# Optimization experiments

Hardware: AMD Instinct MI355X
Metric: run time of the kernel (lower is better)

The kernel has to match this reference:

```python
import jax, jax.numpy as jnp
import numpy as np

D_MODEL = 1024
N_HEAD = 16
D_K = D_MODEL // N_HEAD


def setup_inputs() -> dict:
    key = jax.random.key(0)
    ks = jax.random.split(key, 11)
    B, S, D = 2, 2048, D_MODEL
    scale = 1.0 / np.sqrt(D)
    inp = {
        "q": jax.random.normal(ks[0], (B, S, D), jnp.float32),
        "k": jax.random.normal(ks[1], (B, S, D), jnp.float32),
        "v": jax.random.normal(ks[2], (B, S, D), jnp.float32),
        "w_q": jax.random.normal(ks[3], (D, D), jnp.float32) * scale,
        "b_q": jnp.zeros((D,), jnp.float32),
        "w_k": jax.random.normal(ks[4], (D, D), jnp.float32) * scale,
        "b_k": jnp.zeros((D,), jnp.float32),
        "w_v": jax.random.normal(ks[5], (D, D), jnp.float32) * scale,
        "b_v": jnp.zeros((D,), jnp.float32),
        "w_o": jax.random.normal(ks[6], (D, D), jnp.float32) * scale,
        "b_o": jnp.zeros((D,), jnp.float32),
    }
    return inp


def _split_heads(x):
    # torch: chunk(n_head, dim=-1) then cat(dim=0) -> [H*B, S, d_k]
    B, S, D = x.shape
    x = x.reshape(B, S, N_HEAD, D_K)            # contiguous last-dim chunks
    return x.transpose(2, 0, 1, 3).reshape(N_HEAD * B, S, D_K)


def _merge_heads(x, B):
    # torch: chunk(n_head, dim=0) then cat(dim=-1) -> [B, S, D]
    HB, S, dk = x.shape
    x = x.reshape(N_HEAD, B, S, dk).transpose(1, 2, 0, 3)
    return x.reshape(B, S, N_HEAD * dk)


def reference(q, k, v, w_q, b_q, w_k, b_k, w_v, b_v, w_o, b_o):
    B = q.shape[0]
    qh = _split_heads(q @ w_q + b_q)            # [H*B, S, d_k]
    kh = _split_heads(k @ w_k + b_k)
    vh = _split_heads(v @ w_v + b_v)
    # scaled dot-product attention (naive, materializes scores)
    scores = jnp.einsum('bqd,bkd->bqk', qh, kh) / jnp.sqrt(jnp.float32(D_K))
    attn = jax.nn.softmax(scores, axis=-1)
    out = jnp.einsum('bqk,bkd->bqd', attn, vh)  # [H*B, S, d_k]
    out = _merge_heads(out, B)                  # [B, S, D]
    return out @ w_o + b_o
```

## Files before the change

### kernel.cpp

```cpp
#include <hip/hip_runtime.h>
#include <hip/hip_bf16.h>
#include <stdint.h>

#define DEVINL __device__ __forceinline__

typedef __attribute__((ext_vector_type(8))) short bf16x8;
typedef __attribute__((ext_vector_type(4))) short short4v;
typedef __attribute__((ext_vector_type(8))) unsigned short ushort8;
typedef __attribute__((ext_vector_type(4))) float f32x4;
typedef __attribute__((ext_vector_type(16))) float f32x16;

DEVINL unsigned short f2bf(float x) {
  union { float f; uint32_t u; } v; v.f = x;
  uint32_t u = v.u;
  u += 0x7fffu + ((u >> 16) & 1u);
  return (unsigned short)(u >> 16);
}

DEVINL uint32_t pack_bf16x2(float lo, float hi) {
  __hip_bfloat162 bb = __float22bfloat162_rn(make_float2(lo, hi));
  uint32_t r;
  __builtin_memcpy(&r, &bb, 4);
  return r;
}

DEVINL void gload_lds16(const void* g, void* l) {
  __builtin_amdgcn_global_load_lds((const __attribute__((address_space(1))) void*)g,
                                   (__attribute__((address_space(3))) void*)l, 16, 0, 0);
}

#define E2(x) __builtin_amdgcn_exp2f(x)

__global__ void cvt3_f32_bf16(const float* __restrict__ in0, unsigned short* __restrict__ out0,
                              const float* __restrict__ in1, unsigned short* __restrict__ out1,
                              const float* __restrict__ in2, unsigned short* __restrict__ out2,
                              int nper) {
  int nblk = gridDim.x / 3;
  int which = blockIdx.x / nblk;
  int i = ((blockIdx.x % nblk) * blockDim.x + threadIdx.x) * 8;
  if (i >= nper) return;
  const float* in = which == 0 ? in0 : which == 1 ? in1 : in2;
  unsigned short* out = which == 0 ? out0 : which == 1 ? out1 : out2;
  float4 a = *(const float4*)(in + i);
  float4 b = *(const float4*)(in + i + 4);
  ushort8 r;
  r[0] = f2bf(a.x); r[1] = f2bf(a.y); r[2] = f2bf(a.z); r[3] = f2bf(a.w);
  r[4] = f2bf(b.x); r[5] = f2bf(b.y); r[6] = f2bf(b.z); r[7] = f2bf(b.w);
  *(ushort8*)(out + i) = r;
}

__global__ __launch_bounds__(256) void transpose_w4(
    const float* __restrict__ w0, unsigned short* __restrict__ o0,
    const float* __restrict__ w1, unsigned short* __restrict__ o1,
    const float* __restrict__ w2, unsigned short* __restrict__ o2,
    const float* __restrict__ w3, unsigned short* __restrict__ o3) {
  __shared__ float tile[64][65];
  int z = blockIdx.z;
  const float* w = z == 0 ? w0 : z == 1 ? w1 : z == 2 ? w2 : w3;
  unsigned short* wt = z == 0 ? o0 : z == 1 ? o1 : z == 2 ? o2 : o3;
  int k0 = blockIdx.y * 64, n0 = blockIdx.x * 64;
  int t = threadIdx.x;
  for (int i = 0; i < 4; ++i) {
    int r = (t >> 4) + i * 16;
    int c = (t & 15) * 4;
    float4 v = *(const float4*)(w + (size_t)(k0 + r) * 1024 + n0 + c);
    tile[r][c] = v.x; tile[r][c + 1] = v.y; tile[r][c + 2] = v.z; tile[r][c + 3] = v.w;
  }
  __syncthreads();
  for (int i = 0; i < 4; ++i) {
    int rn = (t >> 4) + i * 16;
    int ck = (t & 15) * 4;
    short4v o;
    o[0] = (short)f2bf(tile[ck + 0][rn]);
    o[1] = (short)f2bf(tile[ck + 1][rn]);
    o[2] = (short)f2bf(tile[ck + 2][rn]);
    o[3] = (short)f2bf(tile[ck + 3][rn]);
    *(short4v*)(wt + (size_t)(n0 + rn) * 1024 + k0 + ck) = o;
  }
}

DEVINL void gemm_body(const unsigned short* __restrict__ A,
                      const unsigned short* __restrict__ Bt,
                      const float* __restrict__ bias,
                      void* __restrict__ out, float scale, int mode,
                      int bx, int by) {
  constexpr int K = 1024;
  __shared__ unsigned short Alds[2 * 128 * 32];
  __shared__ unsigned short Blds[2 * 64 * 32];
  int tile_m = bx * 128;
  int tile_n = by * 64;
  int t = threadIdx.x, lane = t & 63, wid = t >> 6;
  int wm = wid >> 1, wn = wid & 1;
  int fr = lane & 15, fq = lane >> 4;
  f32x4 acc[4][2] = {};

  int ga0 = wid * 64 + lane, ga1 = ga0 + 256;
  int gb0 = wid * 64 + lane;
  int ra0 = ga0 >> 2, ca0 = ((ga0 & 3) ^ ((ra0 >> 1) & 3)) * 8;
  int ra1 = ga1 >> 2, ca1 = ((ga1 & 3) ^ ((ra1 >> 1) & 3)) * 8;
  int rb0 = gb0 >> 2, cb0 = ((gb0 & 3) ^ ((rb0 >> 1) & 3)) * 8;
  const unsigned short* Abase = A  + (size_t)tile_m * K;
  const unsigned short* Bbase = Bt + (size_t)tile_n * K;

  int aoff[4], boff[2];
#pragma unroll
  for (int i = 0; i < 4; ++i) {
    int r = wm * 64 + i * 16 + fr;
    aoff[i] = (r * 4 + (fq ^ ((r >> 1) & 3))) * 8;
  }
#pragma unroll
  for (int j = 0; j < 2; ++j) {
    int r = wn * 32 + j * 16 + fr;
    boff[j] = (r * 4 + (fq ^ ((r >> 1) & 3))) * 8;
  }

  auto stage = [&](int nb, int k0) {
    gload_lds16(Abase + (size_t)ra0 * K + k0 + ca0, Alds + nb * 4096 + ga0 * 8);
    gload_lds16(Abase + (size_t)ra1 * K + k0 + ca1, Alds + nb * 4096 + ga1 * 8);
    gload_lds16(Bbase + (size_t)rb0 * K + k0 + cb0, Blds + nb * 2048 + gb0 * 8);
  };
  auto compute = [&](int nb) {
    bf16x8 af[4], bfb[2];
#pragma unroll
    for (int i = 0; i < 4; ++i) af[i] = *(const bf16x8*)(Alds + nb * 4096 + aoff[i]);
#pragma unroll
    for (int j = 0; j < 2; ++j) bfb[j] = *(const bf16x8*)(Blds + nb * 2048 + boff[j]);
#pragma unroll
    for (int i = 0; i < 4; ++i)
#pragma unroll
      for (int j = 0; j < 2; ++j)
        acc[i][j] = __builtin_amdgcn_mfma_f32_16x16x32_bf16(af[i], bfb[j], acc[i][j], 0, 0, 0);
  };

  stage(0, 0);
  __syncthreads();
  for (int it = 0; it < 16; ++it) {
    int k1 = (2 * it + 1) * 32, k2 = (2 * it + 2) * 32;
    stage(1, k1);
    compute(0);
    __syncthreads();
    if (k2 < K) stage(0, k2);
    compute(1);
    __syncthreads();
  }

#pragma unroll
  for (int i = 0; i < 4; ++i) {
#pragma unroll
    for (int j = 0; j < 2; ++j) {
      int n = tile_n + wn * 32 + j * 16 + fr;
      float bv = bias[n];
      int m0 = tile_m + wm * 64 + i * 16 + fq * 4;
      if (mode == 0) {
        size_t base = (size_t)((n >> 6) * 2 + (m0 >> 11)) * (2048 * 64) + (n & 63);
#pragma unroll
        for (int r = 0; r < 4; ++r)
          ((unsigned short*)out)[base + (size_t)((m0 + r) & 2047) * 64] =
              f2bf((acc[i][j][r] + bv) * scale);
      } else if (mode == 2) {
        size_t base = (size_t)((n >> 6) * 2 + (m0 >> 11)) * (64 * 2048)
                    + (size_t)(n & 63) * 2048 + (m0 & 2047);
        short4v o;
#pragma unroll
        for (int r = 0; r < 4; ++r) o[r] = (short)f2bf(acc[i][j][r] + bv);
        *(short4v*)((unsigned short*)out + base) = o;
      } else {
#pragma unroll
        for (int r = 0; r < 4; ++r)
          ((float*)out)[(size_t)(m0 + r) * 1024 + n] = acc[i][j][r] + bv;
      }
    }
  }
}

__global__ __launch_bounds__(256) void gemm_qkv(
    const unsigned short* __restrict__ Xq, const unsigned short* __restrict__ Xk,
    const unsigned short* __restrict__ Xv,
    const unsigned short* __restrict__ Wtq, const unsigned short* __restrict__ Wtk,
    const unsigned short* __restrict__ Wtv,
    const float* __restrict__ bq, const float* __restrict__ bk,
    const float* __restrict__ bv,
    unsigned short* __restrict__ Qh, unsigned short* __restrict__ Kh,
    unsigned short* __restrict__ Vt, float qscale) {
  int z = blockIdx.z;
  const unsigned short* A  = z == 0 ? Xq : z == 1 ? Xk : Xv;
  const unsigned short* Bt = z == 0 ? Wtq : z == 1 ? Wtk : Wtv;
  const float* bias        = z == 0 ? bq : z == 1 ? bk : bv;
  void* out                = z == 0 ? (void*)Qh : z == 1 ? (void*)Kh : (void*)Vt;
  float scale = z == 0 ? qscale : 1.0f;
  int mode = z == 2 ? 2 : 0;
  gemm_body(A, Bt, bias, out, scale, mode, blockIdx.x, blockIdx.y);
}

__global__ __launch_bounds__(256) void gemm_o(
    const unsigned short* __restrict__ A, const unsigned short* __restrict__ Bt,
    const float* __restrict__ bias, float* __restrict__ out) {
  gemm_body(A, Bt, bias, out, 1.0f, 1, blockIdx.x, blockIdx.y);
}

__global__ __launch_bounds__(256) void attn_fwd(
    const unsigned short* __restrict__ Qh,
    const unsigned short* __restrict__ Kh,
    const unsigned short* __restrict__ Vtg,
    unsigned short* __restrict__ O) {
  constexpr int S = 2048, DK = 64;
  __shared__ unsigned short Klds[2 * 64 * 64];
  __shared__ unsigned short Vlds[2 * 64 * 64];
  __shared__ unsigned short Plds[4 * 32 * 72];

  int wg = blockIdx.x;
  int swz = (wg & 7) * 64 + (wg >> 3);
  int hb = swz >> 4;
  int qt = swz & 15;
  int t = threadIdx.x, lane = t & 63, wid = t >> 6;
  int lq = lane & 31, hi = lane >> 5;
  int q0 = qt * 128;

  const unsigned short* Qb = Qh  + (size_t)hb * S * DK;
  const unsigned short* Kb = Kh  + (size_t)hb * S * DK;
  const unsigned short* Vb = Vtg + (size_t)hb * DK * S;

  bf16x8 qf[4];
#pragma unroll
  for (int kk = 0; kk < 4; ++kk)
    qf[kk] = *(const bf16x8*)(Qb + (size_t)(q0 + wid * 32 + lq) * DK + kk * 16 + hi * 8);

  int g0 = wid * 128 + lane, g1 = g0 + 64;
  int sr0 = g0 >> 3, sc0 = ((g0 & 7) ^ (sr0 & 7)) * 8;
  int sr1 = g1 >> 3, sc1 = ((g1 & 7) ^ (sr1 & 7)) * 8;

  int koff[2][4], voff[2][4];
#pragma unroll
  for (int h2 = 0; h2 < 2; ++h2) {
    int row = 32 * h2 + lq;
#pragma unroll
    for (int kk = 0; kk < 4; ++kk)
      koff[h2][kk] = (row * 8 + ((2 * kk + hi) ^ (row & 7))) * 8;
  }
#pragma unroll
  for (int jt = 0; jt < 2; ++jt) {
    int row = 32 * jt + lq;
#pragma unroll
    for (int ks = 0; ks < 4; ++ks)
      voff[jt][ks] = (row * 8 + ((2 * ks + hi) ^ (row & 7))) * 8;
  }

  unsigned short* Pw = Plds + wid * (32 * 72) + lq * 72;

  auto stage = [&](int nb, int kt) {
    const unsigned short* Ksrc = Kb + (size_t)kt * 64 * DK;
    const unsigned short* Vsrc = Vb + (size_t)kt * 64;
    gload_lds16(Ksrc + sr0 * 64 + sc0, Klds + nb * 4096 + g0 * 8);
    gload_lds16(Ksrc + sr1 * 64 + sc1, Klds + nb * 4096 + g1 * 8);
    gload_lds16(Vsrc + (size_t)sr0 * S + sc0, Vlds + nb * 4096 + g0 * 8);
    gload_lds16(Vsrc + (size_t)sr1 * S + sc1, Vlds + nb * 4096 + g1 * 8);
  };

  float m = -INFINITY, l = 0.f;
  f32x16 oacc[2] = {};

  auto tilestep = [&](int nb) {
    const unsigned short* Kc = Klds + nb * 4096;
    const unsigned short* Vc = Vlds + nb * 4096;

    f32x16 sacc[2] = {};
#pragma unroll
    for (int kk = 0; kk < 4; ++kk) {
      bf16x8 k0 = *(const bf16x8*)(Kc + koff[0][kk]);
      sacc[0] = __builtin_amdgcn_mfma_f32_32x32x16_bf16(k0, qf[kk], sacc[0], 0, 0, 0);
      bf16x8 k1 = *(const bf16x8*)(Kc + koff[1][kk]);
      sacc[1] = __builtin_amdgcn_mfma_f32_32x32x16_bf16(k1, qf[kk], sacc[1], 0, 0, 0);
    }

    float pmax = fmaxf(sacc[0][0], sacc[0][1]);
#pragma unroll
    for (int r = 2; r < 16; r += 2) pmax = fmaxf(pmax, fmaxf(sacc[0][r], sacc[0][r + 1]));
#pragma unroll
    for (int r = 0; r < 16; r += 2) pmax = fmaxf(pmax, fmaxf(sacc[1][r], sacc[1][r + 1]));
    pmax = fmaxf(pmax, __shfl_xor(pmax, 32, 64));

    if (!__all(pmax <= m + 8.0f)) {
      float mn = fmaxf(m, pmax);
      float cf = E2(m - mn);
      m = mn;
      l *= cf;
#pragma unroll
      for (int jt = 0; jt < 2; ++jt)
#pragma unroll
        for (int r = 0; r < 16; ++r) oacc[jt][r] *= cf;
    }

    float ps[4] = {0.f, 0.f, 0.f, 0.f};
#pragma unroll
    for (int r = 0; r < 16; ++r) {
      float p0 = E2(sacc[0][r] - m);
      float p1 = E2(sacc[1][r] - m);
      sacc[0][r] = p0; sacc[1][r] = p1;
      ps[r & 3] += p0 + p1;
    }
    float psum = (ps[0] + ps[1]) + (ps[2] + ps[3]);
    psum += __shfl_xor(psum, 32, 64);
    l += psum;

#pragma unroll
    for (int h2 = 0; h2 < 2; ++h2)
#pragma unroll
      for (int rp = 0; rp < 8; ++rp) {
        uint32_t w = pack_bf16x2(sacc[h2][2 * rp], sacc[h2][2 * rp + 1]);
        int key = 32 * h2 + 8 * (rp >> 1) + 4 * hi + 2 * (rp & 1);
        *(uint32_t*)(Pw + key) = w;
      }
    bf16x8 pfrag[4];
#pragma unroll
    for (int ks = 0; ks < 4; ++ks)
      pfrag[ks] = *(const bf16x8*)(Pw + 16 * ks + 8 * hi);

#pragma unroll
    for (int jt = 0; jt < 2; ++jt)
#pragma unroll
      for (int ks = 0; ks < 4; ++ks) {
        bf16x8 vf = *(const bf16x8*)(Vc + voff[jt][ks]);
        oacc[jt] = __builtin_amdgcn_mfma_f32_32x32x16_bf16(vf, pfrag[ks], oacc[jt], 0, 0, 0);
      }
  };

  stage(0, 0);
  __syncthreads();
  for (int it = 0; it < 16; ++it) {
    int t1 = 2 * it + 1, t2 = 2 * it + 2;
    stage(1, t1);
    tilestep(0);
    __syncthreads();
    if (t2 < 32) stage(0, t2);
    tilestep(1);
    __syncthreads();
  }

  int h = hb >> 1, b = hb & 1;
  int q = q0 + wid * 32 + lq;
  float linv = 1.0f / l;
  unsigned short* orow = O + (size_t)(b * 2048 + q) * 1024 + h * 64;
#pragma unroll
  for (int jt = 0; jt < 2; ++jt)
#pragma unroll
    for (int g = 0; g < 4; ++g) {
      short4v o;
#pragma unroll
      for (int r = 0; r < 4; ++r) o[r] = (short)f2bf(oacc[jt][4 * g + r] * linv);
      *(short4v*)(orow + jt * 32 + 8 * g + 4 * hi) = o;
    }
}

extern "C" void kernel_launch(void* const* d_in, const int* in_sizes, int n_in,
                              void* d_out, int out_size, void* d_ws, size_t ws_size,
                              hipStream_t stream) {
  const float* q   = (const float*)d_in[0];
  const float* k   = (const float*)d_in[1];
  const float* v   = (const float*)d_in[2];
  const float* w_q = (const float*)d_in[3];
  const float* b_q = (const float*)d_in[4];
  const float* w_k = (const float*)d_in[5];
  const float* b_k = (const float*)d_in[6];
  const float* w_v = (const float*)d_in[7];
  const float* b_v = (const float*)d_in[8];
  const float* w_o = (const float*)d_in[9];
  const float* b_o = (const float*)d_in[10];

  char* ws = (char*)d_ws;
  unsigned short* Xq  = (unsigned short*)(ws + 0);
  unsigned short* Xk  = (unsigned short*)(ws + 8388608);
  unsigned short* Xv  = (unsigned short*)(ws + 16777216);
  unsigned short* Wtq = (unsigned short*)(ws + 25165824);
  unsigned short* Wtk = (unsigned short*)(ws + 27262976);
  unsigned short* Wtv = (unsigned short*)(ws + 29360128);
  unsigned short* Wto = (unsigned short*)(ws + 31457280);
  unsigned short* Qh  = (unsigned short*)(ws + 33554432);
  unsigned short* Kh  = (unsigned short*)(ws + 41943040);
  unsigned short* Vt  = (unsigned short*)(ws + 50331648);
  unsigned short* Obuf = Xq;

  const int NACT = 4096 * 1024;
  cvt3_f32_bf16<<<3 * (NACT / 8 / 256), 256, 0, stream>>>(q, Xq, k, Xk, v, Xv, NACT);

  dim3 tg(16, 16, 4);
  transpose_w4<<<tg, 256, 0, stream>>>(w_q, Wtq, w_k, Wtk, w_v, Wtv, w_o, Wto);

  const float qscale = 0.125f * 1.44269504088896340736f;
  dim3 gq(32, 16, 3);
  gemm_qkv<<<gq, 256, 0, stream>>>(Xq, Xk, Xv, Wtq, Wtk, Wtv,
                                   b_q, b_k, b_v, Qh, Kh, Vt, qscale);

  attn_fwd<<<512, 256, 0, stream>>>(Qh, Kh, Vt, Obuf);

  dim3 gg(32, 16);
  gemm_o<<<gg, 256, 0, stream>>>(Obuf, Wto, b_o, (float*)d_out);
}
```

Baseline: 146.2 us.

## Keep two global-to-LDS loads in flight using partial vmcnt waits

```diff
diff --git a/kernel.cpp b/kernel.cpp
--- a/kernel.cpp
+++ b/kernel.cpp
@@ -30,6 +30,13 @@
 }
 
 #define E2(x) __builtin_amdgcn_exp2f(x)
+
+DEVINL void barrier_raw() {
+  asm volatile("" ::: "memory");
+  __builtin_amdgcn_s_barrier();
+  asm volatile("" ::: "memory");
+}
+#define WAITVM(N) asm volatile("s_waitcnt vmcnt(" #N ")" ::: "memory")
 
 __global__ void cvt3_f32_bf16(const float* __restrict__ in0, unsigned short* __restrict__ out0,
                               const float* __restrict__ in1, unsigned short* __restrict__ out1,
@@ -133,16 +140,26 @@
   };
 
   stage(0, 0);
-  __syncthreads();
-  for (int it = 0; it < 16; ++it) {
-    int k1 = (2 * it + 1) * 32, k2 = (2 * it + 2) * 32;
-    stage(1, k1);
+  stage(1, 32);
+  WAITVM(3);
+  barrier_raw();
+  for (int it = 0; it < 15; ++it) {
     compute(0);
-    __syncthreads();
-    if (k2 < K) stage(0, k2);
+    barrier_raw();
+    stage(0, 64 * it + 64);
+    WAITVM(3);
+    barrier_raw();
     compute(1);
-    __syncthreads();
-  }
+    barrier_raw();
+    stage(1, 64 * it + 96);
+    WAITVM(3);
+    barrier_raw();
+  }
+  compute(0);
+  barrier_raw();
+  WAITVM(0);
+  barrier_raw();
+  compute(1);
 
 #pragma unroll
   for (int i = 0; i < 4; ++i) {
@@ -325,16 +342,26 @@
   };
 
   stage(0, 0);
-  __syncthreads();
-  for (int it = 0; it < 16; ++it) {
-    int t1 = 2 * it + 1, t2 = 2 * it + 2;
-    stage(1, t1);
+  stage(1, 1);
+  WAITVM(4);
+  barrier_raw();
+  for (int it = 0; it < 15; ++it) {
     tilestep(0);
-    __syncthreads();
-    if (t2 < 32) stage(0, t2);
+    barrier_raw();
+    stage(0, 2 * it + 2);
+    WAITVM(4);
+    barrier_raw();
     tilestep(1);
-    __syncthreads();
-  }
+    barrier_raw();
+    stage(1, 2 * it + 3);
+    WAITVM(4);
+    barrier_raw();
+  }
+  tilestep(0);
+  barrier_raw();
+  WAITVM(0);
+  barrier_raw();
+  tilestep(1);
 
   int h = hb >> 1, b = hb & 1;
   int q = q0 + wid * 32 + lq;
```

After: 146.2 us. No clear change (+0.0%).

## Enlarge GEMM tiles to 128x128, keep P in registers, add MFMA priority hints

Applied to the files above, without the earlier changes.

```diff
diff --git a/kernel.cpp b/kernel.cpp
--- a/kernel.cpp
+++ b/kernel.cpp
@@ -9,6 +9,7 @@
 typedef __attribute__((ext_vector_type(8))) unsigned short ushort8;
 typedef __attribute__((ext_vector_type(4))) float f32x4;
 typedef __attribute__((ext_vector_type(16))) float f32x16;
+typedef __attribute__((ext_vector_type(4))) int int4v;
 
 DEVINL unsigned short f2bf(float x) {
   union { float f; uint32_t u; } v; v.f = x;
@@ -17,9 +18,9 @@
   return (unsigned short)(u >> 16);
 }
 
-DEVINL uint32_t pack_bf16x2(float lo, float hi) {
+DEVINL int pack_bf16x2(float lo, float hi) {
   __hip_bfloat162 bb = __float22bfloat162_rn(make_float2(lo, hi));
-  uint32_t r;
+  int r;
   __builtin_memcpy(&r, &bb, 4);
   return r;
 }
@@ -86,49 +87,48 @@
                       int bx, int by) {
   constexpr int K = 1024;
   __shared__ unsigned short Alds[2 * 128 * 32];
-  __shared__ unsigned short Blds[2 * 64 * 32];
+  __shared__ unsigned short Blds[2 * 128 * 32];
   int tile_m = bx * 128;
-  int tile_n = by * 64;
+  int tile_n = by * 128;
   int t = threadIdx.x, lane = t & 63, wid = t >> 6;
   int wm = wid >> 1, wn = wid & 1;
   int fr = lane & 15, fq = lane >> 4;
-  f32x4 acc[4][2] = {};
-
-  int ga0 = wid * 64 + lane, ga1 = ga0 + 256;
-  int gb0 = wid * 64 + lane;
-  int ra0 = ga0 >> 2, ca0 = ((ga0 & 3) ^ ((ra0 >> 1) & 3)) * 8;
-  int ra1 = ga1 >> 2, ca1 = ((ga1 & 3) ^ ((ra1 >> 1) & 3)) * 8;
-  int rb0 = gb0 >> 2, cb0 = ((gb0 & 3) ^ ((rb0 >> 1) & 3)) * 8;
+  f32x4 acc[4][4] = {};
+
+  int g0 = wid * 64 + lane, g1 = g0 + 256;
+  int r0 = g0 >> 2, c0 = ((g0 & 3) ^ ((r0 >> 1) & 3)) * 8;
+  int r1 = g1 >> 2, c1 = ((g1 & 3) ^ ((r1 >> 1) & 3)) * 8;
   const unsigned short* Abase = A  + (size_t)tile_m * K;
   const unsigned short* Bbase = Bt + (size_t)tile_n * K;
 
-  int aoff[4], boff[2];
+  int aoff[4], boff[4];
 #pragma unroll
   for (int i = 0; i < 4; ++i) {
     int r = wm * 64 + i * 16 + fr;
     aoff[i] = (r * 4 + (fq ^ ((r >> 1) & 3))) * 8;
   }
 #pragma unroll
-  for (int j = 0; j < 2; ++j) {
-    int r = wn * 32 + j * 16 + fr;
+  for (int j = 0; j < 4; ++j) {
+    int r = wn * 64 + j * 16 + fr;
     boff[j] = (r * 4 + (fq ^ ((r >> 1) & 3))) * 8;
   }
 
   auto stage = [&](int nb, int k0) {
-    gload_lds16(Abase + (size_t)ra0 * K + k0 + ca0, Alds + nb * 4096 + ga0 * 8);
-    gload_lds16(Abase + (size_t)ra1 * K + k0 + ca1, Alds + nb * 4096 + ga1 * 8);
-    gload_lds16(Bbase + (size_t)rb0 * K + k0 + cb0, Blds + nb * 2048 + gb0 * 8);
+    gload_lds16(Abase + (size_t)r0 * K + k0 + c0, Alds + nb * 4096 + g0 * 8);
+    gload_lds16(Abase + (size_t)r1 * K + k0 + c1, Alds + nb * 4096 + g1 * 8);
+    gload_lds16(Bbase + (size_t)r0 * K + k0 + c0, Blds + nb * 4096 + g0 * 8);
+    gload_lds16(Bbase + (size_t)r1 * K + k0 + c1, Blds + nb * 4096 + g1 * 8);
   };
   auto compute = [&](int nb) {
-    bf16x8 af[4], bfb[2];
+    bf16x8 af[4], bfb[4];
 #pragma unroll
     for (int i = 0; i < 4; ++i) af[i] = *(const bf16x8*)(Alds + nb * 4096 + aoff[i]);
 #pragma unroll
-    for (int j = 0; j < 2; ++j) bfb[j] = *(const bf16x8*)(Blds + nb * 2048 + boff[j]);
+    for (int j = 0; j < 4; ++j) bfb[j] = *(const bf16x8*)(Blds + nb * 4096 + boff[j]);
 #pragma unroll
     for (int i = 0; i < 4; ++i)
 #pragma unroll
-      for (int j = 0; j < 2; ++j)
+      for (int j = 0; j < 4; ++j)
         acc[i][j] = __builtin_amdgcn_mfma_f32_16x16x32_bf16(af[i], bfb[j], acc[i][j], 0, 0, 0);
   };
 
@@ -144,11 +144,12 @@
     __syncthreads();
   }
 
+  int fqs = ((fq & 1) << 1) | (fq >> 1);
 #pragma unroll
   for (int i = 0; i < 4; ++i) {
 #pragma unroll
-    for (int j = 0; j < 2; ++j) {
-      int n = tile_n + wn * 32 + j * 16 + fr;
+    for (int j = 0; j < 4; ++j) {
+      int n = tile_n + wn * 64 + j * 16 + fr;
       float bv = bias[n];
       int m0 = tile_m + wm * 64 + i * 16 + fq * 4;
       if (mode == 0) {
@@ -158,8 +159,9 @@
           ((unsigned short*)out)[base + (size_t)((m0 + r) & 2047) * 64] =
               f2bf((acc[i][j][r] + bv) * scale);
       } else if (mode == 2) {
+        int m0s = tile_m + wm * 64 + i * 16 + fqs * 4;
         size_t base = (size_t)((n >> 6) * 2 + (m0 >> 11)) * (64 * 2048)
-                    + (size_t)(n & 63) * 2048 + (m0 & 2047);
+                    + (size_t)(n & 63) * 2048 + (m0s & 2047);
         short4v o;
 #pragma unroll
         for (int r = 0; r < 4; ++r) o[r] = (short)f2bf(acc[i][j][r] + bv);
@@ -206,7 +208,6 @@
   constexpr int S = 2048, DK = 64;
   __shared__ unsigned short Klds[2 * 64 * 64];
   __shared__ unsigned short Vlds[2 * 64 * 64];
-  __shared__ unsigned short Plds[4 * 32 * 72];
 
   int wg = blockIdx.x;
   int swz = (wg & 7) * 64 + (wg >> 3);
@@ -244,8 +245,6 @@
     for (int ks = 0; ks < 4; ++ks)
       voff[jt][ks] = (row * 8 + ((2 * ks + hi) ^ (row & 7))) * 8;
   }
-
-  unsigned short* Pw = Plds + wid * (32 * 72) + lq * 72;
 
   auto stage = [&](int nb, int kt) {
     const unsigned short* Ksrc = Kb + (size_t)kt * 64 * DK;
@@ -264,6 +263,7 @@
     const unsigned short* Vc = Vlds + nb * 4096;
 
     f32x16 sacc[2] = {};
+    __builtin_amdgcn_s_setprio(1);
 #pragma unroll
     for (int kk = 0; kk < 4; ++kk) {
       bf16x8 k0 = *(const bf16x8*)(Kc + koff[0][kk]);
@@ -271,6 +271,7 @@
       bf16x8 k1 = *(const bf16x8*)(Kc + koff[1][kk]);
       sacc[1] = __builtin_amdgcn_mfma_f32_32x32x16_bf16(k1, qf[kk], sacc[1], 0, 0, 0);
     }
+    __builtin_amdgcn_s_setprio(0);
 
     float pmax = fmaxf(sacc[0][0], sacc[0][1]);
 #pragma unroll
@@ -302,19 +303,19 @@
     psum += __shfl_xor(psum, 32, 64);
     l += psum;
 
-#pragma unroll
-    for (int h2 = 0; h2 < 2; ++h2)
-#pragma unroll
-      for (int rp = 0; rp < 8; ++rp) {
-        uint32_t w = pack_bf16x2(sacc[h2][2 * rp], sacc[h2][2 * rp + 1]);
-        int key = 32 * h2 + 8 * (rp >> 1) + 4 * hi + 2 * (rp & 1);
-        *(uint32_t*)(Pw + key) = w;
-      }
     bf16x8 pfrag[4];
 #pragma unroll
-    for (int ks = 0; ks < 4; ++ks)
-      pfrag[ks] = *(const bf16x8*)(Pw + 16 * ks + 8 * hi);
-
+    for (int ks = 0; ks < 4; ++ks) {
+      const int h2 = ks >> 1, b = 8 * (ks & 1);
+      int4v w;
+      w[0] = pack_bf16x2(sacc[h2][b + 0], sacc[h2][b + 1]);
+      w[1] = pack_bf16x2(sacc[h2][b + 2], sacc[h2][b + 3]);
+      w[2] = pack_bf16x2(sacc[h2][b + 4], sacc[h2][b + 5]);
+      w[3] = pack_bf16x2(sacc[h2][b + 6], sacc[h2][b + 7]);
+      pfrag[ks] = __builtin_bit_cast(bf16x8, w);
+    }
+
+    __builtin_amdgcn_s_setprio(1);
 #pragma unroll
     for (int jt = 0; jt < 2; ++jt)
 #pragma unroll
@@ -322,6 +323,7 @@
         bf16x8 vf = *(const bf16x8*)(Vc + voff[jt][ks]);
         oacc[jt] = __builtin_amdgcn_mfma_f32_32x32x16_bf16(vf, pfrag[ks], oacc[jt], 0, 0, 0);
       }
+    __builtin_amdgcn_s_setprio(0);
   };
 
   stage(0, 0);
@@ -386,12 +388,12 @@
   transpose_w4<<<tg, 256, 0, stream>>>(w_q, Wtq, w_k, Wtk, w_v, Wtv, w_o, Wto);
 
   const float qscale = 0.125f * 1.44269504088896340736f;
-  dim3 gq(32, 16, 3);
+  dim3 gq(32, 8, 3);
   gemm_qkv<<<gq, 256, 0, stream>>>(Xq, Xk, Xv, Wtq, Wtk, Wtv,
                                    b_q, b_k, b_v, Qh, Kh, Vt, qscale);
 
   attn_fwd<<<512, 256, 0, stream>>>(Qh, Kh, Vt, Obuf);
 
-  dim3 gg(32, 16);
+  dim3 gg(32, 8);
   gemm_o<<<gg, 256, 0, stream>>>(Obuf, Wto, b_o, (float*)d_out);
 }
```

Result: slower. 155.7 us (+6.5%).
